# Optimization experiments

Measured on AMD Instinct MI355X. Metric: run time of the kernel, lower is better.

Reference implementation:

```python
import jax, jax.numpy as jnp
import numpy as np

EPS = 1e-5
NUM_GROUPS = 32


def group_norm(x, scale, bias):
    # x: [B, C, H, W], 32 groups, normalized over (C/G, H, W)
    B, C, H, W = x.shape
    G = NUM_GROUPS
    xg = x.reshape(B, G, C // G, H, W)
    mean = xg.mean(axis=(2, 3, 4), keepdims=True)
    var = xg.var(axis=(2, 3, 4), keepdims=True)
    xg = (xg - mean) * jax.lax.rsqrt(var + EPS)
    x = xg.reshape(B, C, H, W)
    return x * scale[None, :, None, None] + bias[None, :, None, None]


def setup_inputs() -> dict:
    key = jax.random.key(0)
    ks = jax.random.split(key, 6)
    B, C, H, W = 32, 512, 32, 32
    std = 1.0 / np.sqrt(C)
    return {
        "x": jax.random.normal(ks[0], (B, C, H, W), dtype=jnp.float32),
        "gn_scale": jnp.ones((C,), dtype=jnp.float32),
        "gn_bias": jnp.zeros((C,), dtype=jnp.float32),
        "wq": jax.random.normal(ks[1], (C, C), dtype=jnp.float32) * std,
        "bq": jnp.zeros((C,), dtype=jnp.float32),
        "wk": jax.random.normal(ks[2], (C, C), dtype=jnp.float32) * std,
        "bk": jnp.zeros((C,), dtype=jnp.float32),
        "wv": jax.random.normal(ks[3], (C, C), dtype=jnp.float32) * std,
        "bv": jnp.zeros((C,), dtype=jnp.float32),
        "wo": jax.random.normal(ks[4], (C, C), dtype=jnp.float32) * std,
        "bo": jnp.zeros((C,), dtype=jnp.float32),
    }


def reference(x, gn_scale, gn_bias, wq, bq, wk, bk, wv, bv, wo, bo):
    B, C, H, W = x.shape
    h = group_norm(x, gn_scale, gn_bias)
    # 1x1 convs == per-pixel matmuls; flatten spatial to tokens: [B, HW, C]
    ht = h.reshape(B, C, H * W).transpose(0, 2, 1)
    q = jnp.einsum('bnc,oc->bno', ht, wq) + bq  # [B, HW, C]
    k = jnp.einsum('bnc,oc->bno', ht, wk) + bk
    v = jnp.einsum('bnc,oc->bno', ht, wv) + bv
    scale = 1.0 / jnp.sqrt(jnp.asarray(C, x.dtype))
    w = jnp.einsum('bnc,bmc->bnm', q, k) * scale  # [B, HW, HW]
    w = jax.nn.softmax(w, axis=-1)
    a = jnp.einsum('bnm,bmc->bnc', w, v)  # [B, HW, C]
    out = jnp.einsum('bnc,oc->bno', a, wo) + bo
    out = out.transpose(0, 2, 1).reshape(B, C, H, W)
    return x + out
```

## Files before the change

### kernel.cpp

```cpp
#include <hip/hip_runtime.h>
#include <stdint.h>

typedef unsigned short u16;
typedef __attribute__((ext_vector_type(8))) short short8;
typedef __attribute__((ext_vector_type(4))) float f32x4;

#define NTOK 1024
#define CDIM 512
#define NG 32

#define GLOAD_LDS16(gptr, lptr)                                                              \
  __builtin_amdgcn_global_load_lds((const __attribute__((address_space(1))) unsigned int*)(gptr), \
                                   (__attribute__((address_space(3))) unsigned int*)(lptr), 16, 0, 0)

__device__ __forceinline__ u16 f2bf(float f) {
  union { float f; uint32_t u; } v; v.f = f;
  uint32_t r = v.u + 0x7fffu + ((v.u >> 16) & 1u);
  return (u16)(r >> 16);
}

__device__ __forceinline__ float bf2f(u16 b) {
  union { uint32_t u; float f; } v; v.u = ((uint32_t)b) << 16;
  return v.f;
}

__global__ __launch_bounds__(256) void wconv(const float* __restrict__ wq, const float* __restrict__ wk,
                                             const float* __restrict__ wv, const float* __restrict__ wo,
                                             const float* __restrict__ bq, const float* __restrict__ bk,
                                             u16* __restrict__ out, float* __restrict__ bqk) {
  int i = blockIdx.x * 256 + threadIdx.x;
  out[i]          = f2bf(wq[i]);
  out[262144 + i] = f2bf(wk[i]);
  out[524288 + i] = f2bf(wv[i]);
  out[786432 + i] = f2bf(wo[i]);
  if (i < 512) bqk[i] = bq[i];
  else if (i < 1024) bqk[i] = bk[i - 512];
}

__global__ __launch_bounds__(256) void gn_stats(const float* __restrict__ x,
                                                float* __restrict__ mean_o, float* __restrict__ rstd_o) {
  int bg = blockIdx.x;
  const float4* base = (const float4*)(x + (size_t)bg * 16384);
  float s = 0.f, ss = 0.f;
  for (int i = threadIdx.x; i < 4096; i += 256) {
    float4 v = base[i];
    s  += v.x + v.y + v.z + v.w;
    ss += v.x * v.x + v.y * v.y + v.z * v.z + v.w * v.w;
  }
#pragma unroll
  for (int d = 1; d < 64; d <<= 1) { s += __shfl_xor(s, d); ss += __shfl_xor(ss, d); }
  __shared__ float as[4], as2[4];
  int w = threadIdx.x >> 6;
  if ((threadIdx.x & 63) == 0) { as[w] = s; as2[w] = ss; }
  __syncthreads();
  if (threadIdx.x == 0) {
    float S = as[0] + as[1] + as[2] + as[3];
    float SS = as2[0] + as2[1] + as2[2] + as2[3];
    float m = S * (1.f / 16384.f);
    float var = SS * (1.f / 16384.f) - m * m;
    mean_o[bg] = m;
    rstd_o[bg] = rsqrtf(var + 1e-5f);
  }
}

__global__ __launch_bounds__(256) void gn_apply(const float* __restrict__ x,
                                                const float* __restrict__ mean_, const float* __restrict__ rstd_,
                                                const float* __restrict__ gsc, const float* __restrict__ gbi,
                                                u16* __restrict__ h) {
  int n0 = blockIdx.x * 64, c0 = blockIdx.y * 64, b = blockIdx.z;
  __shared__ u16 t[64][65];
  int tid = threadIdx.x;
  int nl4 = (tid & 15) * 4;
  int clb = tid >> 4;
#pragma unroll
  for (int p = 0; p < 4; ++p) {
    int cl = p * 16 + clb;
    int c = c0 + cl;
    int g = c >> 4;
    float m = mean_[b * NG + g], rs = rstd_[b * NG + g];
    float sc = gsc[c] * rs, bi = gbi[c] - m * sc;
    float4 v = *(const float4*)(x + ((size_t)b * CDIM + c) * NTOK + n0 + nl4);
    t[cl][nl4 + 0] = f2bf(v.x * sc + bi);
    t[cl][nl4 + 1] = f2bf(v.y * sc + bi);
    t[cl][nl4 + 2] = f2bf(v.z * sc + bi);
    t[cl][nl4 + 3] = f2bf(v.w * sc + bi);
  }
  __syncthreads();
  int nl = tid >> 3;
  int cc = (tid & 7) * 8;
#pragma unroll
  for (int p = 0; p < 2; ++p) {
    int n = nl + p * 32;
    short8 o;
#pragma unroll
    for (int i = 0; i < 8; ++i) o[i] = (short)t[cc + i][n];
    *(short8*)(h + (size_t)(b * NTOK + n0 + n) * CDIM + c0 + cc) = o;
  }
}

template <int MODE>
__global__ __launch_bounds__(512, 2) void gemm_nt(const u16* __restrict__ A, const u16* __restrict__ B,
                                                  const float* __restrict__ bias, u16* __restrict__ outb,
                                                  float* __restrict__ outf, const float* __restrict__ resid,
                                                  int Ka, int Kb, int nkt,
                                                  size_t strideA, size_t strideB, int batch0) {
  int nx = gridDim.x, ny = gridDim.y;
  int nwg = nx * ny * gridDim.z;
  int id = blockIdx.x + nx * (blockIdx.y + ny * blockIdx.z);
  int cpx = nwg >> 3;
  int sw = (id & 7) * cpx + (id >> 3);
  int bx = sw % nx; int t_ = sw / nx;
  int by = t_ % ny; int z = t_ / ny;

  const u16* Amat = A + (size_t)z * strideA;
  const u16* Bmat = B + (size_t)z * strideB;
  int n0 = bx * 256, m0 = by * 256;
  __shared__ u16 As[2][16384];
  __shared__ u16 Bs[2][16384];
  int tid = threadIdx.x;
  int l = tid & 63, wid = tid >> 6;
  int lr = l & 15, lh = l >> 4;
  int wm = (wid >> 2) * 128;
  int wn = (wid & 3) * 64;

  f32x4 acc[8][4];
#pragma unroll
  for (int i = 0; i < 8; ++i)
#pragma unroll
    for (int j = 0; j < 4; ++j) acc[i][j] = (f32x4){0.f, 0.f, 0.f, 0.f};

#define STAGE(bufsel, ktv)                                                                \
  {                                                                                       \
    u16* sa = &As[bufsel][0];                                                             \
    u16* sb = &Bs[bufsel][0];                                                             \
    _Pragma("unroll")                                                                     \
    for (int i_ = 0; i_ < 4; ++i_) {                                                      \
      int u_ = tid + 512 * i_;                                                            \
      int row_ = u_ >> 3, lc_ = u_ & 7;                                                   \
      int gcol_ = ((lc_ ^ (row_ & 7)) << 3);                                              \
      GLOAD_LDS16(Amat + (size_t)(m0 + row_) * Ka + (ktv) * 64 + gcol_, sa + row_ * 64 + lc_ * 8); \
      GLOAD_LDS16(Bmat + (size_t)(n0 + row_) * Kb + (ktv) * 64 + gcol_, sb + row_ * 64 + lc_ * 8); \
    }                                                                                     \
  }

#define COMPUTE(bufsel)                                                                   \
  {                                                                                       \
    const u16* ca = &As[bufsel][0];                                                       \
    const u16* cb = &Bs[bufsel][0];                                                       \
    _Pragma("unroll")                                                                     \
    for (int ks = 0; ks < 2; ++ks) {                                                      \
      short8 af[8], bfr[4];                                                               \
      _Pragma("unroll")                                                                   \
      for (int i_ = 0; i_ < 8; ++i_) {                                                    \
        int row_ = wm + i_ * 16 + lr;                                                     \
        int u_ = (ks * 4 + lh) ^ (row_ & 7);                                              \
        af[i_] = *(const short8*)(ca + row_ * 64 + u_ * 8);                               \
      }                                                                                   \
      _Pragma("unroll")                                                                   \
      for (int j_ = 0; j_ < 4; ++j_) {                                                    \
        int row_ = wn + j_ * 16 + lr;                                                     \
        int u_ = (ks * 4 + lh) ^ (row_ & 7);                                              \
        bfr[j_] = *(const short8*)(cb + row_ * 64 + u_ * 8);                              \
      }                                                                                   \
      _Pragma("unroll")                                                                   \
      for (int i_ = 0; i_ < 8; ++i_)                                                      \
        _Pragma("unroll")                                                                 \
        for (int j_ = 0; j_ < 4; ++j_)                                                    \
          acc[i_][j_] = __builtin_amdgcn_mfma_f32_16x16x32_bf16(af[i_], bfr[j_], acc[i_][j_], 0, 0, 0); \
    }                                                                                     \
  }

  STAGE(0, 0);
  __syncthreads();
  int cur = 0;
  for (int kt = 0; kt < nkt - 1; ++kt) {
    STAGE(cur ^ 1, kt + 1);
    __builtin_amdgcn_sched_barrier(0);
    COMPUTE(cur);
    __syncthreads();
    cur ^= 1;
  }
  COMPUTE(cur);

#pragma unroll
  for (int i = 0; i < 8; ++i)
#pragma unroll
    for (int j = 0; j < 4; ++j)
#pragma unroll
      for (int r = 0; r < 4; ++r) {
        int gr = m0 + wm + i * 16 + lh * 4 + r;
        int gc = n0 + wn + j * 16 + lr;
        float v = acc[i][j][r];
        if (MODE == 0) {
          v += bias[gc];
          outb[(size_t)gr * 1024 + gc] = f2bf(v);
        } else if (MODE == 1 || MODE == 2) {
          v += bias[gr];
          int bt = gc >> 10, nn = gc & 1023;
          size_t addr = ((size_t)bt * 512 + gr) * 1024 + nn;
          if (MODE == 1) outb[addr] = f2bf(v);
          else outf[addr] = v + resid[addr];
        } else if (MODE == 3) {
          outb[((size_t)z * 1024 + gr) * 1024 + gc] = f2bf(v);
        } else {
          outb[((size_t)((batch0 + z) * 1024 + gr)) * 512 + gc] = f2bf(v);
        }
      }
#undef STAGE
#undef COMPUTE
}

__global__ __launch_bounds__(256) void softmax_rows(u16* __restrict__ S) {
  const float scale = 0.04419417382415922f;
  int row = blockIdx.x * 4 + (threadIdx.x >> 6);
  int l = threadIdx.x & 63;
  u16* Sr = S + (size_t)row * 1024;
  short8 a = *(const short8*)(Sr + l * 8);
  short8 b = *(const short8*)(Sr + 512 + l * 8);
  float f[16];
#pragma unroll
  for (int i = 0; i < 8; ++i) { f[i] = bf2f((u16)a[i]); f[8 + i] = bf2f((u16)b[i]); }
  float mx = f[0];
#pragma unroll
  for (int i = 1; i < 16; ++i) mx = fmaxf(mx, f[i]);
#pragma unroll
  for (int d = 1; d < 64; d <<= 1) mx = fmaxf(mx, __shfl_xor(mx, d));
  float s = 0.f;
#pragma unroll
  for (int i = 0; i < 16; ++i) { f[i] = __expf((f[i] - mx) * scale); s += f[i]; }
#pragma unroll
  for (int d = 1; d < 64; d <<= 1) s += __shfl_xor(s, d);
  float inv = 1.f / s;
  short8 oa, ob;
#pragma unroll
  for (int i = 0; i < 8; ++i) { oa[i] = (short)f2bf(f[i] * inv); ob[i] = (short)f2bf(f[8 + i] * inv); }
  *(short8*)(Sr + l * 8) = oa;
  *(short8*)(Sr + 512 + l * 8) = ob;
}

extern "C" void kernel_launch(void* const* d_in, const int* in_sizes, int n_in,
                              void* d_out, int out_size, void* d_ws, size_t ws_size,
                              hipStream_t stream) {
  const float* x   = (const float*)d_in[0];
  const float* gsc = (const float*)d_in[1];
  const float* gbi = (const float*)d_in[2];
  const float* wq  = (const float*)d_in[3];
  const float* bq  = (const float*)d_in[4];
  const float* wk  = (const float*)d_in[5];
  const float* bk  = (const float*)d_in[6];
  const float* wv  = (const float*)d_in[7];
  const float* bv  = (const float*)d_in[8];
  const float* wo  = (const float*)d_in[9];
  const float* bo  = (const float*)d_in[10];

  char* ws = (char*)d_ws;
  u16* wbf = (u16*)ws;
  float* bqk = (float*)(ws + (2ull << 20));
  float* mean_ = (float*)(ws + (2ull << 20) + 65536);
  float* rstd_ = mean_ + 1024;
  u16* h   = (u16*)(ws + (4ull << 20));
  u16* qk  = (u16*)(ws + (36ull << 20));
  u16* vm  = (u16*)(ws + (100ull << 20));
  u16* S   = (u16*)(ws + (132ull << 20));
  u16* am  = h;
  float* out = (float*)d_out;

  size_t sbytes = ws_size > (132ull << 20) ? ws_size - (132ull << 20) : 0;
  int CB = 1;
  while (CB < 32 && (size_t)(CB * 2) * (2ull << 20) <= sbytes) CB *= 2;

  wconv<<<1024, 256, 0, stream>>>(wq, wk, wv, wo, bq, bk, wbf, bqk);
  gn_stats<<<1024, 256, 0, stream>>>(x, mean_, rstd_);
  gn_apply<<<dim3(16, 8, 32), 256, 0, stream>>>(x, mean_, rstd_, gsc, gbi, h);
  gemm_nt<0><<<dim3(4, 128), 512, 0, stream>>>(h, wbf, bqk, qk, nullptr, nullptr,
                                               512, 512, 8, 0, 0, 0);
  gemm_nt<1><<<dim3(128, 2), 512, 0, stream>>>(wbf + 524288, h, bv, vm, nullptr, nullptr,
                                               512, 512, 8, 0, 0, 0);
  for (int c0 = 0; c0 < 32; c0 += CB) {
    gemm_nt<3><<<dim3(4, 4, CB), 512, 0, stream>>>(qk + (size_t)c0 * 1048576, qk + 512 + (size_t)c0 * 1048576,
                                                   nullptr, S, nullptr, nullptr,
                                                   1024, 1024, 8, 1048576, 1048576, 0);
    softmax_rows<<<CB * 256, 256, 0, stream>>>(S);
    gemm_nt<4><<<dim3(2, 4, CB), 512, 0, stream>>>(S, vm + (size_t)c0 * 524288,
                                                   nullptr, am, nullptr, nullptr,
                                                   1024, 1024, 16, 1048576, 524288, c0);
  }
  gemm_nt<2><<<dim3(128, 2), 512, 0, stream>>>(wbf + 786432, am, bo, nullptr, out, x,
                                               512, 512, 8, 0, 0, 0);
}
```

Before: 262.8 us.

## Rework GEMM main loop into four-phase half-tile pipeline with priority hints

```diff
diff --git a/kernel.cpp b/kernel.cpp
--- a/kernel.cpp
+++ b/kernel.cpp
@@ -129,58 +129,114 @@
 #pragma unroll
     for (int j = 0; j < 4; ++j) acc[i][j] = (f32x4){0.f, 0.f, 0.f, 0.f};
 
-#define STAGE(bufsel, ktv)                                                                \
-  {                                                                                       \
-    u16* sa = &As[bufsel][0];                                                             \
-    u16* sb = &Bs[bufsel][0];                                                             \
-    _Pragma("unroll")                                                                     \
-    for (int i_ = 0; i_ < 4; ++i_) {                                                      \
-      int u_ = tid + 512 * i_;                                                            \
-      int row_ = u_ >> 3, lc_ = u_ & 7;                                                   \
-      int gcol_ = ((lc_ ^ (row_ & 7)) << 3);                                              \
-      GLOAD_LDS16(Amat + (size_t)(m0 + row_) * Ka + (ktv) * 64 + gcol_, sa + row_ * 64 + lc_ * 8); \
-      GLOAD_LDS16(Bmat + (size_t)(n0 + row_) * Kb + (ktv) * 64 + gcol_, sb + row_ * 64 + lc_ * 8); \
-    }                                                                                     \
-  }
-
-#define COMPUTE(bufsel)                                                                   \
-  {                                                                                       \
-    const u16* ca = &As[bufsel][0];                                                       \
-    const u16* cb = &Bs[bufsel][0];                                                       \
-    _Pragma("unroll")                                                                     \
-    for (int ks = 0; ks < 2; ++ks) {                                                      \
-      short8 af[8], bfr[4];                                                               \
-      _Pragma("unroll")                                                                   \
-      for (int i_ = 0; i_ < 8; ++i_) {                                                    \
-        int row_ = wm + i_ * 16 + lr;                                                     \
-        int u_ = (ks * 4 + lh) ^ (row_ & 7);                                              \
-        af[i_] = *(const short8*)(ca + row_ * 64 + u_ * 8);                               \
-      }                                                                                   \
-      _Pragma("unroll")                                                                   \
-      for (int j_ = 0; j_ < 4; ++j_) {                                                    \
-        int row_ = wn + j_ * 16 + lr;                                                     \
-        int u_ = (ks * 4 + lh) ^ (row_ & 7);                                              \
-        bfr[j_] = *(const short8*)(cb + row_ * 64 + u_ * 8);                              \
-      }                                                                                   \
-      _Pragma("unroll")                                                                   \
-      for (int i_ = 0; i_ < 8; ++i_)                                                      \
-        _Pragma("unroll")                                                                 \
-        for (int j_ = 0; j_ < 4; ++j_)                                                    \
-          acc[i_][j_] = __builtin_amdgcn_mfma_f32_16x16x32_bf16(af[i_], bfr[j_], acc[i_][j_], 0, 0, 0); \
-    }                                                                                     \
-  }
-
-  STAGE(0, 0);
-  __syncthreads();
-  int cur = 0;
-  for (int kt = 0; kt < nkt - 1; ++kt) {
-    STAGE(cur ^ 1, kt + 1);
-    __builtin_amdgcn_sched_barrier(0);
-    COMPUTE(cur);
-    __syncthreads();
-    cur ^= 1;
-  }
-  COMPUTE(cur);
+  short8 af[4][2];
+  short8 bf01[2][2];
+  short8 bf23[2][2];
+
+  int sr = tid >> 3, sc = tid & 7;
+  int sg = (sc ^ (sr & 7)) << 3;
+  const u16* Ag0 = Amat + (size_t)(m0 + sr) * Ka + sg;
+  const u16* Ag1 = Ag0 + (size_t)64 * Ka;
+  const u16* Bg0 = Bmat + (size_t)(n0 + sr) * Kb + sg;
+  const u16* Bg1 = Bg0 + (size_t)64 * Kb;
+  size_t hA = (size_t)128 * Ka, hB = (size_t)128 * Kb;
+  u16* Al0 = &As[0][sr * 64 + sc * 8];
+  u16* Bl0 = &Bs[0][sr * 64 + sc * 8];
+
+#define STAGE_A(bufsel, ktv, half)                                        \
+  {                                                                       \
+    size_t go_ = (size_t)(ktv) * 64 + ((half) ? hA : (size_t)0);          \
+    u16* ld_ = Al0 + (bufsel) * 16384 + (half) * 8192;                    \
+    GLOAD_LDS16(Ag0 + go_, ld_);                                          \
+    GLOAD_LDS16(Ag1 + go_, ld_ + 4096);                                   \
+  }
+#define STAGE_B(bufsel, ktv, half)                                        \
+  {                                                                       \
+    size_t go_ = (size_t)(ktv) * 64 + ((half) ? hB : (size_t)0);          \
+    u16* ld_ = Bl0 + (bufsel) * 16384 + (half) * 8192;                    \
+    GLOAD_LDS16(Bg0 + go_, ld_);                                          \
+    GLOAD_LDS16(Bg1 + go_, ld_ + 4096);                                   \
+  }
+
+#define READ_AF(ihalf, bufsel)                                                        \
+  _Pragma("unroll") for (int i_ = 0; i_ < 4; ++i_) {                                  \
+    int row_ = wm + (ihalf) * 64 + i_ * 16 + lr;                                      \
+    const u16* p_ = &As[bufsel][row_ * 64];                                           \
+    _Pragma("unroll") for (int ks_ = 0; ks_ < 2; ++ks_)                               \
+      af[i_][ks_] = *(const short8*)(p_ + (((ks_ * 4 + lh) ^ (row_ & 7)) << 3));      \
+  }
+
+#define READ_BF(dst, jbase, bufsel)                                                   \
+  _Pragma("unroll") for (int j_ = 0; j_ < 2; ++j_) {                                  \
+    int row_ = wn + ((jbase) + j_) * 16 + lr;                                         \
+    const u16* p_ = &Bs[bufsel][row_ * 64];                                           \
+    _Pragma("unroll") for (int ks_ = 0; ks_ < 2; ++ks_)                               \
+      dst[j_][ks_] = *(const short8*)(p_ + (((ks_ * 4 + lh) ^ (row_ & 7)) << 3));     \
+  }
+
+#define MFMA_Q(ihalf, jbase, bsrc)                                                    \
+  _Pragma("unroll") for (int ks_ = 0; ks_ < 2; ++ks_)                                 \
+    _Pragma("unroll") for (int i_ = 0; i_ < 4; ++i_)                                  \
+      _Pragma("unroll") for (int j_ = 0; j_ < 2; ++j_)                                \
+        acc[(ihalf) * 4 + i_][(jbase) + j_] = __builtin_amdgcn_mfma_f32_16x16x32_bf16( \
+            af[i_][ks_], bsrc[j_][ks_], acc[(ihalf) * 4 + i_][(jbase) + j_], 0, 0, 0);
+
+#define PBAR() asm volatile("s_barrier" ::: "memory")
+
+#define PHASES(BC, BN, GI, DOHI, DOLO)                                    \
+  {                                                                       \
+    int g1_ = (GI) + 1, g2_ = (GI) + 2;                                   \
+                                           \
+    READ_AF(0, BC);                                                       \
+    READ_BF(bf01, 0, BC);                                                 \
+    if (DOHI) { STAGE_A(BN, g1_, 1); }                                    \
+    PBAR();                                                               \
+    __builtin_amdgcn_s_setprio(1);                                        \
+    MFMA_Q(0, 0, bf01);                                                   \
+    __builtin_amdgcn_s_setprio(0);                                        \
+    PBAR();                                                               \
+                                           \
+    READ_BF(bf23, 2, BC);                                                 \
+    if (DOHI) { STAGE_B(BN, g1_, 1); }                                    \
+    PBAR();                                                               \
+    __builtin_amdgcn_s_setprio(1);                                        \
+    MFMA_Q(0, 2, bf23);                                                   \
+    __builtin_amdgcn_s_setprio(0);                                        \
+    PBAR();                                                               \
+     \
+    READ_AF(1, BC);                                                       \
+    if (DOLO) { STAGE_B(BC, g2_, 0); }                                    \
+    PBAR();                                                               \
+    __builtin_amdgcn_s_setprio(1);                                        \
+    MFMA_Q(1, 2, bf23);                                                   \
+    __builtin_amdgcn_s_setprio(0);                                        \
+    PBAR();                                                               \
+     \
+    if (DOLO) { STAGE_A(BC, g2_, 0); }                                    \
+    PBAR();                                                               \
+    __builtin_amdgcn_s_setprio(1);                                        \
+    MFMA_Q(1, 0, bf01);                                                   \
+    __builtin_amdgcn_s_setprio(0);                                        \
+    if (DOLO) { asm volatile("s_waitcnt vmcnt(4)" ::: "memory"); }        \
+    else      { asm volatile("s_waitcnt vmcnt(0)" ::: "memory"); }        \
+    PBAR();                                                               \
+  }
+
+  int k1 = (1 < nkt) ? 1 : 0;
+  STAGE_B(0, 0, 0);
+  STAGE_A(0, 0, 0);
+  STAGE_A(0, 0, 1);
+  STAGE_B(0, 0, 1);
+  STAGE_B(1, k1, 0);
+  STAGE_A(1, k1, 0);
+  asm volatile("s_waitcnt vmcnt(4)" ::: "memory");
+  PBAR();
+
+  for (int kt = 0; kt < nkt; kt += 2) {
+    int more = (kt + 2 < nkt) ? 1 : 0;
+    PHASES(0, 1, kt, 1, more);
+    PHASES(1, 0, kt + 1, more, more);
+  }
 
 #pragma unroll
   for (int i = 0; i < 8; ++i)
@@ -206,8 +262,13 @@
           outb[((size_t)((batch0 + z) * 1024 + gr)) * 512 + gc] = f2bf(v);
         }
       }
-#undef STAGE
-#undef COMPUTE
+#undef STAGE_A
+#undef STAGE_B
+#undef READ_AF
+#undef READ_BF
+#undef MFMA_Q
+#undef PBAR
+#undef PHASES
 }
 
 __global__ __launch_bounds__(256) void softmax_rows(u16* __restrict__ S) {
```

After: 261.9 us. About the same (-0.3%).
